# Kernel optimization log

Measured on AMD Instinct MI355X. Metric: run time of the kernel, lower is better.

Reference implementation:

```python
import jax, jax.numpy as jnp
from jax import lax
import numpy as np

PATCH = 16
FREQ = 8
TWO_PI = 2.0 * np.pi


def setup_inputs() -> dict:
    key = jax.random.key(0)
    ks = jax.random.split(key, 4)
    B, C, H, W = 8, 64, 128, 128
    E, O, HID = 8, 64, 128
    GATE_C = C + 4 * FREQ  # 96
    x = jax.random.normal(ks[0], (B, C, H, W), dtype=jnp.float32)
    We = jax.random.normal(ks[1], (E, O, C, 3, 3), dtype=jnp.float32) * (1.0 / np.sqrt(C * 9))
    be = jnp.zeros((E, O), dtype=jnp.float32)
    W1 = jax.random.normal(ks[2], (HID, GATE_C), dtype=jnp.float32) * (1.0 / np.sqrt(GATE_C))
    b1 = jnp.zeros((HID,), dtype=jnp.float32)
    W2 = jax.random.normal(ks[3], (E, HID), dtype=jnp.float32) * (1.0 / np.sqrt(HID))
    b2 = jnp.zeros((E,), dtype=jnp.float32)
    return {"x": x, "We": We, "be": be, "W1": W1, "b1": b1, "W2": W2, "b2": b2}


def _fourier_grid(nH, nW, dtype):
    # positional Fourier features of patch centers: [4*FREQ, nH, nW]
    u = (jnp.arange(nH, dtype=dtype) + 0.5) / nH
    v = (jnp.arange(nW, dtype=dtype) + 0.5) / nW
    uu, vv = jnp.meshgrid(u, v, indexing="ij")  # [nH,nW]
    freqs = (2.0 ** jnp.arange(FREQ, dtype=dtype))[:, None, None]
    au = TWO_PI * freqs * uu[None]
    av = TWO_PI * freqs * vv[None]
    return jnp.concatenate([jnp.sin(au), jnp.cos(au), jnp.sin(av), jnp.cos(av)], axis=0)


def reference(x, We, be, W1, b1, W2, b2):
    B, C, H, W = x.shape
    E = We.shape[0]
    P = PATCH
    nH, nW = H // P, W // P

    # --- router gate: per-patch pooled channels + fourier positional feats ---
    xp = x.reshape(B, C, nH, P, nW, P).mean(axis=(3, 5))  # [B,C,nH,nW]
    four = _fourier_grid(nH, nW, x.dtype)  # [4F,nH,nW]
    g = jnp.concatenate([xp, jnp.broadcast_to(four, (B,) + four.shape)], axis=1)  # [B,gate_c,nH,nW]
    h = jax.nn.relu(jnp.einsum("hc,bcij->bhij", W1, g) + b1[None, :, None, None])
    logits = jnp.einsum("eh,bhij->beij", W2, h) + b2[None, :, None, None]
    probs = jax.nn.softmax(logits, axis=1)  # [B,E,nH,nW]

    # --- conv experts (3x3, SAME, ReLU; dropout inactive at eval) ---
    def expert(w, b):
        y = lax.conv_general_dilated(x, w, (1, 1), "SAME",
                                     dimension_numbers=("NCHW", "OIHW", "NCHW"))
        return jax.nn.relu(y + b[None, :, None, None])

    y = jax.vmap(expert)(We, be)  # [E,B,O,H,W]

    # --- combine: broadcast patch gates to pixels and weight-sum experts ---
    gates = jnp.repeat(jnp.repeat(probs, P, axis=2), P, axis=3)  # [B,E,H,W]
    out = jnp.einsum("ebchw,behw->bchw", y, gates)
    return out
```

## Files before the change

kernel.cpp:

```cpp
#include <hip/hip_runtime.h>
#include <math.h>

#define BB 8
#define CC 64
#define HH 128
#define WW 128
#define EE 8
#define OO 64
#define HID 128
#define GATEC 96
#define NP 8
#define PP 16

typedef __attribute__((ext_vector_type(8))) short bf16x8;
typedef __attribute__((ext_vector_type(4))) float f32x4;

static __device__ __forceinline__ unsigned short f2bf(float f) {
  unsigned int u = __builtin_bit_cast(unsigned int, f);
  unsigned int r = (u + 0x7FFFu + ((u >> 16) & 1u)) >> 16;
  return (unsigned short)r;
}

__global__ __launch_bounds__(256) void prep_kernel(
    const float* __restrict__ x,
    const float* __restrict__ W1, const float* __restrict__ b1,
    const float* __restrict__ W2, const float* __restrict__ b2,
    const float* __restrict__ We,
    float* __restrict__ probs, unsigned short* __restrict__ wp) {
  __shared__ float ps[256];
  __shared__ float g[GATEC];
  __shared__ float hbuf[HID];
  __shared__ float lg[EE];

  if (blockIdx.x >= 512) {
    int idx = (blockIdx.x - 512) * 256 + threadIdx.x;
    if (idx < EE * 9 * OO * CC) {
      int c  = idx & 63;
      int o  = (idx >> 6) & 63;
      int et = idx >> 12;
      int t  = et % 9;
      int e  = et / 9;
      float v = We[(((size_t)(e * OO + o) * CC) + c) * 9 + t];
      int dst = (et << 12) + (((c >> 5) * 4 + (o >> 4)) << 9)
              + ((((c >> 3) & 3) * 16 + (o & 15)) << 3) + (c & 7);
      wp[dst] = f2bf(v);
    }
    return;
  }

  int blk = blockIdx.x;
  int b  = blk >> 6;
  int pi = (blk >> 3) & 7;
  int pj = blk & 7;
  int t  = threadIdx.x;

  {
    int c = t >> 2, q = t & 3;
    const float* xb = x + ((size_t)(b * CC + c) * HH + pi * PP + q * 4) * WW + pj * PP;
    float s = 0.f;
    for (int r = 0; r < 4; ++r)
      for (int col = 0; col < PP; ++col)
        s += xb[r * WW + col];
    ps[t] = s;
  }
  __syncthreads();
  if (t < CC) {
    g[t] = (ps[4*t] + ps[4*t+1] + ps[4*t+2] + ps[4*t+3]) * (1.f / 256.f);
  } else if (t < CC + 32) {
    int k = t - CC;
    int fi = k & 7, kind = k >> 3;
    float freq  = (float)(1 << fi);
    float coord = (kind < 2) ? ((pi + 0.5f) / 8.f) : ((pj + 0.5f) / 8.f);
    float a = 6.28318530717958647692f * freq * coord;
    g[t] = (kind & 1) ? cosf(a) : sinf(a);
  }
  __syncthreads();
  if (t < HID) {
    float acc = b1[t];
    const float* w = W1 + (size_t)t * GATEC;
    for (int c = 0; c < GATEC; ++c) acc += w[c] * g[c];
    hbuf[t] = fmaxf(acc, 0.f);
  }
  __syncthreads();
  if (t < EE) {
    float acc = b2[t];
    const float* w = W2 + (size_t)t * HID;
    for (int k = 0; k < HID; ++k) acc += w[k] * hbuf[k];
    lg[t] = acc;
  }
  __syncthreads();
  if (t < EE) {
    float m = lg[0];
    for (int e = 1; e < EE; ++e) m = fmaxf(m, lg[e]);
    float sum = 0.f;
    for (int e = 0; e < EE; ++e) sum += expf(lg[e] - m);
    probs[((size_t)(b * EE + t) * NP + pi) * NP + pj] = expf(lg[t] - m) / sum;
  }
}

__global__ __launch_bounds__(256, 2) void conv_moe(
    const float* __restrict__ x,
    const unsigned short* __restrict__ wp,
    const float* __restrict__ be,
    const float* __restrict__ probs, float* __restrict__ out) {
  int bx0 = blockIdx.x;
  int b   = blockIdx.y;
  int rg = bx0 >> 2, cg = bx0 & 3;
  const int h0 = rg * 8, w0 = cg * 32;
  const int pi = rg >> 1;
  const int pj0 = cg * 2;

  int lane = threadIdx.x & 63;
  int wave = threadIdx.x >> 6;
  int px   = lane & 15;
  int kg   = lane >> 4;

  __shared__ char xs[340 * 128];

  for (int idx = threadIdx.x; idx < 340 * 8; idx += 256) {
    int j  = idx / 340;
    int sp = idx % 340;
    int r = sp / 34, col = sp % 34;
    int gr = h0 + r - 1, gc = w0 + col - 1;
    bf16x8 v;
    if (gr >= 0 && gr < HH && gc >= 0 && gc < WW) {
      const float* xb = x + ((size_t)(b * CC + j * 8) * HH + gr) * WW + gc;
#pragma unroll
      for (int q = 0; q < 8; ++q) v[q] = (short)f2bf(xb[(size_t)q * HH * WW]);
    } else {
#pragma unroll
      for (int q = 0; q < 8; ++q) v[q] = 0;
    }
    int g = (gr + gc) & 7;
    *(bf16x8*)(xs + sp * 128 + ((j ^ g) & 7) * 16) = v;
  }
  __syncthreads();

  f32x4 outacc[4][4], acc[4][4];
#pragma unroll
  for (int ot = 0; ot < 4; ++ot)
#pragma unroll
    for (int f = 0; f < 4; ++f) { outacc[ot][f] = (f32x4)(0.f); acc[ot][f] = (f32x4)(0.f); }

  const int gl = h0 + w0 - 2 + wave * 2 + px;

  const unsigned short* wq = wp + lane * 8;

#define LOADW(bank, tap)                                                        \
  {                                                                             \
    const unsigned short* wt_ = wq + (size_t)(tap) * 4096;                      \
    _Pragma("unroll")                                                           \
    for (int i = 0; i < 8; ++i)                                                 \
      bank[i] = *(const bf16x8*)(wt_ + i * 512);                                \
  }

#define LOADBX(dst, dy, dx, ks)                                                 \
  {                                                                             \
    _Pragma("unroll")                                                           \
    for (int f = 0; f < 4; ++f) {                                               \
      int rowp = f >> 1, ch = f & 1;                                            \
      int sp = (wave * 2 + rowp + (dy)) * 34 + ch * 16 + px + (dx);             \
      int slot = (((((ks) << 2) | kg) ^ (gl + rowp + (dy) + (dx))) & 7);        \
      dst[f] = *(const bf16x8*)(xs + sp * 128 + (slot << 4));                   \
    }                                                                           \
  }

#define TAP(bank, dy, dx)                                                       \
  {                                                                             \
    bf16x8 bx0[4], bx1[4];                                                      \
    LOADBX(bx0, dy, dx, 0);                                                     \
    LOADBX(bx1, dy, dx, 1);                                                     \
    __builtin_amdgcn_s_setprio(1);                                              \
    _Pragma("unroll")                                                           \
    for (int ot = 0; ot < 4; ++ot)                                              \
      _Pragma("unroll")                                                         \
      for (int f = 0; f < 4; ++f)                                               \
        acc[ot][f] = __builtin_amdgcn_mfma_f32_16x16x32_bf16(bank[ot], bx0[f],  \
                                                             acc[ot][f], 0, 0, 0); \
    _Pragma("unroll")                                                           \
    for (int ot = 0; ot < 4; ++ot)                                              \
      _Pragma("unroll")                                                         \
      for (int f = 0; f < 4; ++f)                                               \
        acc[ot][f] = __builtin_amdgcn_mfma_f32_16x16x32_bf16(bank[4 + ot], bx1[f], \
                                                             acc[ot][f], 0, 0, 0); \
    __builtin_amdgcn_s_setprio(0);                                              \
  }

#define EPILOGUE(eidx)                                                          \
  {                                                                             \
    float gA = probs[((size_t)(b * EE + (eidx)) * NP + pi) * NP + pj0];         \
    float gB = probs[((size_t)(b * EE + (eidx)) * NP + pi) * NP + pj0 + 1];     \
    _Pragma("unroll")                                                           \
    for (int ot = 0; ot < 4; ++ot) {                                            \
      f32x4 bias = *(const f32x4*)(be + (eidx) * OO + ot * 16 + kg * 4);        \
      _Pragma("unroll")                                                         \
      for (int f = 0; f < 4; ++f) {                                             \
        float gt = (f & 1) ? gB : gA;                                           \
        _Pragma("unroll")                                                       \
        for (int r = 0; r < 4; ++r) {                                           \
          outacc[ot][f][r] += gt * fmaxf(acc[ot][f][r] + bias[r], 0.f);         \
          acc[ot][f][r] = 0.f;                                                  \
        }                                                                       \
      }                                                                         \
    }                                                                           \
  }

#define ADVANCE()                                                               \
  {                                                                             \
    if (t9 == 8) { EPILOGUE(e); ++e; t9 = 0; dy = 0; dx = 0; }                  \
    else { ++t9; if (++dx == 3) { dx = 0; ++dy; } }                             \
  }

  bf16x8 awA[8], awB[8];
  LOADW(awA, 0);
  LOADW(awB, 1);

  int e = 0, t9 = 0, dy = 0, dx = 0;
  for (int u = 0; u < 36; ++u) {
    TAP(awA, dy, dx);
    if (u < 35) LOADW(awA, 2 * u + 2);
    ADVANCE();
    TAP(awB, dy, dx);
    if (u < 35) LOADW(awB, 2 * u + 3);
    ADVANCE();
  }

#pragma unroll
  for (int ot = 0; ot < 4; ++ot) {
#pragma unroll
    for (int f = 0; f < 4; ++f) {
      int rowp = f >> 1, ch = f & 1;
      int o = ot * 16 + kg * 4;
      int h = h0 + wave * 2 + rowp;
      float* op = out + ((size_t)(b * OO + o) * HH + h) * WW + w0 + ch * 16 + px;
#pragma unroll
      for (int r = 0; r < 4; ++r)
        op[(size_t)r * HH * WW] = outacc[ot][f][r];
    }
  }
#undef LOADW
#undef LOADBX
#undef TAP
#undef EPILOGUE
#undef ADVANCE
}

extern "C" void kernel_launch(void* const* d_in, const int* in_sizes, int n_in,
                              void* d_out, int out_size, void* d_ws, size_t ws_size,
                              hipStream_t stream) {
  const float* x  = (const float*)d_in[0];
  const float* We = (const float*)d_in[1];
  const float* be = (const float*)d_in[2];
  const float* W1 = (const float*)d_in[3];
  const float* b1 = (const float*)d_in[4];
  const float* W2 = (const float*)d_in[5];
  const float* b2 = (const float*)d_in[6];
  float* out = (float*)d_out;

  float* probs = (float*)d_ws;
  unsigned short* wpk = (unsigned short*)((char*)d_ws + 16384);

  prep_kernel<<<dim3(512 + (EE * 9 * OO * CC + 255) / 256), dim3(256), 0, stream>>>(
      x, W1, b1, W2, b2, We, probs, wpk);
  conv_moe<<<dim3(16 * 4, BB), dim3(256), 0, stream>>>(x, wpk, be, probs, out);
}
```

Before: 99.25 us.

## Restructure conv LDS layout to padded channel-planes and fully unroll tap schedule

The shared-memory tile changes from a per-pixel XOR-swizzled layout to channel-group planes padded to 341 entries, so LDS addresses become compile-time offsets from one base pointer and no per-tap swizzle arithmetic is needed. The tap loop with runtime dy/dx/t9 counters is replaced by a fully unrolled per-expert macro that issues two experts per loop iteration with double-buffered weight loads. The first MFMA of each expert starts from a zero accumulator instead of resetting acc in the epilogue. The padding is meant to avoid bank conflicts, but the larger unrolled body may raise register pressure and instruction-cache footprint.

```diff
diff --git a/kernel.cpp b/kernel.cpp
--- a/kernel.cpp
+++ b/kernel.cpp
@@ -115,74 +115,66 @@
   int px   = lane & 15;
   int kg   = lane >> 4;
 
-  __shared__ char xs[340 * 128];
-
-  for (int idx = threadIdx.x; idx < 340 * 8; idx += 256) {
-    int j  = idx / 340;
-    int sp = idx % 340;
-    int r = sp / 34, col = sp % 34;
-    int gr = h0 + r - 1, gc = w0 + col - 1;
-    bf16x8 v;
-    if (gr >= 0 && gr < HH && gc >= 0 && gc < WW) {
-      const float* xb = x + ((size_t)(b * CC + j * 8) * HH + gr) * WW + gc;
-#pragma unroll
-      for (int q = 0; q < 8; ++q) v[q] = (short)f2bf(xb[(size_t)q * HH * WW]);
-    } else {
-#pragma unroll
-      for (int q = 0; q < 8; ++q) v[q] = 0;
+  __shared__ char xs[8 * 341 * 16];
+
+  for (int i = 0; i < 11; ++i) {
+    int idx = i * 256 + threadIdx.x;
+    if (idx < 2720) {
+      int j  = idx / 340;
+      int sp = idx - j * 340;
+      int r = sp / 34, col = sp - r * 34;
+      int gr = h0 + r - 1, gc = w0 + col - 1;
+      bf16x8 v;
+      if (gr >= 0 && gr < HH && gc >= 0 && gc < WW) {
+        const float* xb = x + ((size_t)(b * CC + j * 8) * HH + gr) * WW + gc;
+#pragma unroll
+        for (int q = 0; q < 8; ++q) v[q] = (short)f2bf(xb[(size_t)q * HH * WW]);
+      } else {
+#pragma unroll
+        for (int q = 0; q < 8; ++q) v[q] = 0;
+      }
+      *(bf16x8*)(xs + (j * 341 + sp) * 16) = v;
     }
-    int g = (gr + gc) & 7;
-    *(bf16x8*)(xs + sp * 128 + ((j ^ g) & 7) * 16) = v;
-  }
-  __syncthreads();
-
-  f32x4 outacc[4][4], acc[4][4];
-#pragma unroll
-  for (int ot = 0; ot < 4; ++ot)
-#pragma unroll
-    for (int f = 0; f < 4; ++f) { outacc[ot][f] = (f32x4)(0.f); acc[ot][f] = (f32x4)(0.f); }
-
-  const int gl = h0 + w0 - 2 + wave * 2 + px;
-
+  }
+  __syncthreads();
+
+  const char* lb = xs + (kg * 341 + wave * 68 + px) * 16;
   const unsigned short* wq = wp + lane * 8;
 
-#define LOADW(bank, tap)                                                        \
+  f32x4 outacc[16], acc[16];
+#pragma unroll
+  for (int i = 0; i < 16; ++i) outacc[i] = (f32x4)(0.f);
+  const f32x4 kz = (f32x4)(0.f);
+
+#define LOADW(bank, base, tap)                                                  \
+  { _Pragma("unroll") for (int i_ = 0; i_ < 8; ++i_)                            \
+      bank[i_] = *(const bf16x8*)((base) + (tap) * 4096 + i_ * 512); }
+
+#define LDSRD(ks, rd, ch, dx)                                                   \
+  (*(const bf16x8*)(lb + ((ks) * 1364 + (rd) * 34 + (ch) * 16 + (dx)) * 16))
+
+#define DOTAP(BANK, dy, dx, FIRST)                                              \
   {                                                                             \
-    const unsigned short* wt_ = wq + (size_t)(tap) * 4096;                      \
-    _Pragma("unroll")                                                           \
-    for (int i = 0; i < 8; ++i)                                                 \
-      bank[i] = *(const bf16x8*)(wt_ + i * 512);                                \
-  }
-
-#define LOADBX(dst, dy, dx, ks)                                                 \
-  {                                                                             \
-    _Pragma("unroll")                                                           \
-    for (int f = 0; f < 4; ++f) {                                               \
-      int rowp = f >> 1, ch = f & 1;                                            \
-      int sp = (wave * 2 + rowp + (dy)) * 34 + ch * 16 + px + (dx);             \
-      int slot = (((((ks) << 2) | kg) ^ (gl + rowp + (dy) + (dx))) & 7);        \
-      dst[f] = *(const bf16x8*)(xs + sp * 128 + (slot << 4));                   \
+    bf16x8 b0_[4], b1_[4];                                                      \
+    _Pragma("unroll")                                                           \
+    for (int f_ = 0; f_ < 4; ++f_) {                                            \
+      const int rp_ = f_ >> 1, ch_ = f_ & 1;                                    \
+      b0_[f_] = LDSRD(0, rp_ + (dy), ch_, (dx));                                \
+      b1_[f_] = LDSRD(1, rp_ + (dy), ch_, (dx));                                \
     }                                                                           \
-  }
-
-#define TAP(bank, dy, dx)                                                       \
-  {                                                                             \
-    bf16x8 bx0[4], bx1[4];                                                      \
-    LOADBX(bx0, dy, dx, 0);                                                     \
-    LOADBX(bx1, dy, dx, 1);                                                     \
     __builtin_amdgcn_s_setprio(1);                                              \
     _Pragma("unroll")                                                           \
-    for (int ot = 0; ot < 4; ++ot)                                              \
+    for (int ot_ = 0; ot_ < 4; ++ot_)                                           \
       _Pragma("unroll")                                                         \
-      for (int f = 0; f < 4; ++f)                                               \
-        acc[ot][f] = __builtin_amdgcn_mfma_f32_16x16x32_bf16(bank[ot], bx0[f],  \
-                                                             acc[ot][f], 0, 0, 0); \
-    _Pragma("unroll")                                                           \
-    for (int ot = 0; ot < 4; ++ot)                                              \
+      for (int f_ = 0; f_ < 4; ++f_)                                            \
+        acc[ot_ * 4 + f_] = __builtin_amdgcn_mfma_f32_16x16x32_bf16(            \
+            BANK[ot_], b0_[f_], (FIRST) ? kz : acc[ot_ * 4 + f_], 0, 0, 0);     \
+    _Pragma("unroll")                                                           \
+    for (int ot_ = 0; ot_ < 4; ++ot_)                                           \
       _Pragma("unroll")                                                         \
-      for (int f = 0; f < 4; ++f)                                               \
-        acc[ot][f] = __builtin_amdgcn_mfma_f32_16x16x32_bf16(bank[4 + ot], bx1[f], \
-                                                             acc[ot][f], 0, 0, 0); \
+      for (int f_ = 0; f_ < 4; ++f_)                                            \
+        acc[ot_ * 4 + f_] = __builtin_amdgcn_mfma_f32_16x16x32_bf16(            \
+            BANK[4 + ot_], b1_[f_], acc[ot_ * 4 + f_], 0, 0, 0);                \
     __builtin_amdgcn_s_setprio(0);                                              \
   }
 
@@ -191,38 +183,45 @@
     float gA = probs[((size_t)(b * EE + (eidx)) * NP + pi) * NP + pj0];         \
     float gB = probs[((size_t)(b * EE + (eidx)) * NP + pi) * NP + pj0 + 1];     \
     _Pragma("unroll")                                                           \
-    for (int ot = 0; ot < 4; ++ot) {                                            \
-      f32x4 bias = *(const f32x4*)(be + (eidx) * OO + ot * 16 + kg * 4);        \
+    for (int ot_ = 0; ot_ < 4; ++ot_) {                                         \
+      f32x4 bias = *(const f32x4*)(be + (eidx) * OO + ot_ * 16 + kg * 4);       \
       _Pragma("unroll")                                                         \
-      for (int f = 0; f < 4; ++f) {                                             \
-        float gt = (f & 1) ? gB : gA;                                           \
+      for (int f_ = 0; f_ < 4; ++f_) {                                          \
+        float gt = (f_ & 1) ? gB : gA;                                          \
         _Pragma("unroll")                                                       \
-        for (int r = 0; r < 4; ++r) {                                           \
-          outacc[ot][f][r] += gt * fmaxf(acc[ot][f][r] + bias[r], 0.f);         \
-          acc[ot][f][r] = 0.f;                                                  \
-        }                                                                       \
+        for (int r_ = 0; r_ < 4; ++r_)                                          \
+          outacc[ot_ * 4 + f_][r_] +=                                           \
+              gt * fmaxf(acc[ot_ * 4 + f_][r_] + bias[r_], 0.f);                \
       }                                                                         \
     }                                                                           \
   }
 
-#define ADVANCE()                                                               \
+#define EXPERT(eidx, B0, B1, wcur, wnext)                                       \
   {                                                                             \
-    if (t9 == 8) { EPILOGUE(e); ++e; t9 = 0; dy = 0; dx = 0; }                  \
-    else { ++t9; if (++dx == 3) { dx = 0; ++dy; } }                             \
+    LOADW(B1, wcur, 1);  DOTAP(B0, 0, 0, true);                                 \
+    LOADW(B0, wcur, 2);  DOTAP(B1, 0, 1, false);                                \
+    LOADW(B1, wcur, 3);  DOTAP(B0, 0, 2, false);                                \
+    LOADW(B0, wcur, 4);  DOTAP(B1, 1, 0, false);                                \
+    LOADW(B1, wcur, 5);  DOTAP(B0, 1, 1, false);                                \
+    LOADW(B0, wcur, 6);  DOTAP(B1, 1, 2, false);                                \
+    LOADW(B1, wcur, 7);  DOTAP(B0, 2, 0, false);                                \
+    LOADW(B0, wcur, 8);  DOTAP(B1, 2, 1, false);                                \
+    LOADW(B1, wnext, 0); DOTAP(B0, 2, 2, false);                                \
+    EPILOGUE(eidx);                                                             \
   }
 
   bf16x8 awA[8], awB[8];
-  LOADW(awA, 0);
-  LOADW(awB, 1);
-
-  int e = 0, t9 = 0, dy = 0, dx = 0;
-  for (int u = 0; u < 36; ++u) {
-    TAP(awA, dy, dx);
-    if (u < 35) LOADW(awA, 2 * u + 2);
-    ADVANCE();
-    TAP(awB, dy, dx);
-    if (u < 35) LOADW(awB, 2 * u + 3);
-    ADVANCE();
+  LOADW(awA, wq, 0);
+
+  const unsigned short* wqe = wq;
+#pragma unroll 1
+  for (int ep = 0; ep < 4; ++ep) {
+    const unsigned short* wq1 = wqe + 9 * 4096;
+    const unsigned short* wq2 = (ep == 3) ? wq : (wq1 + 9 * 4096);
+    int e0 = ep * 2;
+    EXPERT(e0,     awA, awB, wqe, wq1);
+    EXPERT(e0 + 1, awB, awA, wq1, wq2);
+    wqe = wq2;
   }
 
 #pragma unroll
@@ -235,14 +234,14 @@
       float* op = out + ((size_t)(b * OO + o) * HH + h) * WW + w0 + ch * 16 + px;
 #pragma unroll
       for (int r = 0; r < 4; ++r)
-        op[(size_t)r * HH * WW] = outacc[ot][f][r];
+        op[(size_t)r * HH * WW] = outacc[ot * 4 + f][r];
     }
   }
 #undef LOADW
-#undef LOADBX
-#undef TAP
+#undef LDSRD
+#undef DOTAP
 #undef EPILOGUE
-#undef ADVANCE
+#undef EXPERT
 }
 
 extern "C" void kernel_launch(void* const* d_in, const int* in_sizes, int n_in,
```

After: 345.4 us. 3.48x slower.
